# Kernel optimization log

Measured on AMD Instinct MI355X. Metric: run time of the kernel, lower is better.

The kernel has to match this reference:

```python
import jax, jax.numpy as jnp
import numpy as np

N = 100000
E = 1600000
F_IN = 128
F_OUT = 128


def setup_inputs() -> dict:
    key = jax.random.key(0)
    k1, k2, k3, k4, k5, k6 = jax.random.split(key, 6)
    stdv = 1.0 / np.sqrt(F_OUT)
    x = jax.random.normal(k1, (N, F_IN), dtype=jnp.float32)
    edge_row = jax.random.randint(k2, (E,), 0, N, dtype=jnp.int32)
    edge_col = jax.random.randint(k3, (E,), 0, N, dtype=jnp.int32)
    edge_val = jax.random.uniform(k4, (E,), dtype=jnp.float32)
    weight = jax.random.uniform(k5, (F_IN, F_OUT), minval=-stdv, maxval=stdv, dtype=jnp.float32)
    bias = jax.random.uniform(k6, (F_OUT,), minval=-stdv, maxval=stdv, dtype=jnp.float32)
    return {"x": x, "edge_row": edge_row, "edge_col": edge_col,
            "edge_val": edge_val, "weight": weight, "bias": bias}


def reference(x, edge_row, edge_col, edge_val, weight, bias):
    # support = X @ W  -> [N, F_OUT]
    support = jnp.matmul(x, weight)
    # sparse adjacency matmul: out[i] = sum_{e: row[e]==i} val[e] * support[col[e]]
    messages = edge_val[:, None] * support[edge_col]  # [E, F_OUT]
    out = jax.ops.segment_sum(messages, edge_row, num_segments=N)
    return out + bias
```

## Files before the change

### kernel.cpp

```cpp
#include <hip/hip_runtime.h>

#define FDIM 128
#define RPB  128
#define LOG_RPB 7
#define CAP  2560
#define TILE 8192
#define NTHR 256
#define NB_MAX 1024

typedef __attribute__((ext_vector_type(8))) short short8;
typedef __attribute__((ext_vector_type(4))) float f32x4;

__device__ inline unsigned pack_bf16x2(float a, float b) {
    unsigned ua = __float_as_uint(a);
    unsigned ub = __float_as_uint(b);
    ua += 0x7fffu + ((ua >> 16) & 1u);
    ub += 0x7fffu + ((ub >> 16) & 1u);
    return (ua >> 16) | (ub & 0xffff0000u);
}

__global__ __launch_bounds__(256) void w_prep(const float* __restrict__ W,
                                              uint4* __restrict__ Wsw,
                                              int* __restrict__ gfill, int nb) {
    const int id = blockIdx.x * 256 + threadIdx.x;
    if (id < nb) gfill[id] = id * CAP;
    const int c    = id & 127;
    const int kblk = id >> 7;
    unsigned u[4];
#pragma unroll
    for (int h = 0; h < 4; ++h) {
        float f0 = W[(size_t)(kblk * 8 + 2 * h) * FDIM + c];
        float f1 = W[(size_t)(kblk * 8 + 2 * h + 1) * FDIM + c];
        u[h] = pack_bf16x2(f0, f1);
    }
    Wsw[c * 16 + (kblk ^ (c & 7))] = make_uint4(u[0], u[1], u[2], u[3]);
}

__global__ __launch_bounds__(256) void gemm_mfma(const float* __restrict__ X,
                                                 const uint4* __restrict__ Wsw,
                                                 unsigned* __restrict__ Sb, int N) {
    __shared__ uint4 Wl[2048];
    const int t = threadIdx.x;
#pragma unroll
    for (int s = 0; s < 8; ++s) Wl[t + 256 * s] = Wsw[t + 256 * s];
    __syncthreads();

    const int w    = t >> 6;
    const int lane = t & 63;
    const int g    = lane >> 4;
    const int rl   = lane & 15;
    const int row  = blockIdx.x * 64 + 16 * w + rl;

    short8 bfrag[4];
    if (row < N) {
        const float4* X4 = (const float4*)(X + (size_t)row * FDIM);
#pragma unroll
        for (int kk = 0; kk < 4; ++kk) {
            float4 a = X4[kk * 8 + 2 * g];
            float4 b = X4[kk * 8 + 2 * g + 1];
            union { unsigned u[4]; short8 s; } f;
            f.u[0] = pack_bf16x2(a.x, a.y);
            f.u[1] = pack_bf16x2(a.z, a.w);
            f.u[2] = pack_bf16x2(b.x, b.y);
            f.u[3] = pack_bf16x2(b.z, b.w);
            bfrag[kk] = f.s;
        }
    } else {
        union { unsigned u[4]; short8 s; } z;
        z.u[0] = z.u[1] = z.u[2] = z.u[3] = 0;
#pragma unroll
        for (int kk = 0; kk < 4; ++kk) bfrag[kk] = z.s;
    }

    const short8* Wl8 = (const short8*)Wl;
    f32x4 acc[8] = {};
#pragma unroll
    for (int kk = 0; kk < 4; ++kk) {
#pragma unroll
        for (int ct = 0; ct < 8; ++ct) {
            const int c = ct * 16 + rl;
            short8 af = Wl8[c * 16 + ((kk * 4 + g) ^ (c & 7))];
            acc[ct] = __builtin_amdgcn_mfma_f32_16x16x32_bf16(af, bfrag[kk],
                                                              acc[ct], 0, 0, 0);
        }
    }

    if (row < N) {
#pragma unroll
        for (int ct = 0; ct < 8; ++ct) {
            unsigned u0 = pack_bf16x2(acc[ct][0], acc[ct][1]);
            unsigned u1 = pack_bf16x2(acc[ct][2], acc[ct][3]);
            *(uint2*)(Sb + (size_t)row * 64 + ct * 8 + 2 * g) = make_uint2(u0, u1);
        }
    }
}

__global__ __launch_bounds__(256) void binned_scatter(const int* __restrict__ erow,
                                                      const int* __restrict__ ecol,
                                                      const float* __restrict__ eval,
                                                      int* __restrict__ gfill,
                                                      int2* __restrict__ pairs,
                                                      int E, int nb) {
    __shared__ int lcnt[NB_MAX];
    __shared__ int rsv[NB_MAX];
    const int base = blockIdx.x * TILE;
    const int n = min(TILE, E - base);

    for (int i = threadIdx.x; i < nb; i += NTHR) lcnt[i] = 0;
    __syncthreads();

    for (int i = threadIdx.x; i < n; i += NTHR)
        atomicAdd(&lcnt[erow[base + i] >> LOG_RPB], 1);
    __syncthreads();

    for (int b = threadIdx.x; b < nb; b += NTHR) {
        int c = lcnt[b];
        rsv[b] = c ? atomicAdd(&gfill[b], c) : 0;
        lcnt[b] = 0;
    }
    __syncthreads();

    for (int i = threadIdx.x; i < n; i += NTHR) {
        int r = erow[base + i];
        int b = r >> LOG_RPB;
        int slot = rsv[b] + atomicAdd(&lcnt[b], 1);
        if (slot < b * CAP + CAP)
            pairs[slot] = make_int2(ecol[base + i] | ((r & (RPB - 1)) << 17),
                                    __float_as_int(eval[base + i]));
    }
}

__device__ inline void fma8(float* acc, float v, uint4 s) {
    acc[0] += v * __uint_as_float(s.x << 16);
    acc[1] += v * __uint_as_float(s.x & 0xffff0000u);
    acc[2] += v * __uint_as_float(s.y << 16);
    acc[3] += v * __uint_as_float(s.y & 0xffff0000u);
    acc[4] += v * __uint_as_float(s.z << 16);
    acc[5] += v * __uint_as_float(s.z & 0xffff0000u);
    acc[6] += v * __uint_as_float(s.w << 16);
    acc[7] += v * __uint_as_float(s.w & 0xffff0000u);
}

__global__ __launch_bounds__(512) void bucket_gather(const int* __restrict__ gfill,
                                                     const int2* __restrict__ pairs,
                                                     const uint4* __restrict__ Sb4,
                                                     const float* __restrict__ bias,
                                                     float* __restrict__ out, int N) {
    __shared__ int2 stage[CAP];
    __shared__ unsigned cp[CAP];
    __shared__ int lh[RPB], lx[RPB], lf[RPB], rs[RPB], re[RPB];
    const int b   = blockIdx.x;
    const int gb  = b * CAP;
    const int tid = threadIdx.x;
    const int cnt = min(gfill[b] - gb, CAP);

    for (int i = tid; i < cnt; i += 512) stage[i] = pairs[gb + i];
    if (tid < RPB) lh[tid] = 0;
    __syncthreads();

    for (int i = tid; i < cnt; i += 512)
        atomicAdd(&lh[(stage[i].x >> 17) & (RPB - 1)], 1);
    __syncthreads();

    if (tid < RPB) lx[tid] = lh[tid];
    __syncthreads();
    for (int off = 1; off < RPB; off <<= 1) {
        int y = 0;
        if (tid < RPB && tid >= off) y = lx[tid - off];
        __syncthreads();
        if (tid < RPB) lx[tid] += y;
        __syncthreads();
    }
    if (tid < RPB) {
        int excl = lx[tid] - lh[tid];
        rs[tid] = excl;
        re[tid] = lx[tid];
        lf[tid] = excl;
    }
    __syncthreads();

    for (int i = tid; i < cnt; i += 512) {
        int2 p = stage[i];
        int rl = (p.x >> 17) & (RPB - 1);
        int pos = atomicAdd(&lf[rl], 1);
        int q = __float2int_rn(__int_as_float(p.y) * 32768.f);
        q = min(max(q, 0), 32767);
        cp[pos] = (unsigned)(p.x & 0x1FFFF) | ((unsigned)q << 17);
    }
    __syncthreads();

    const int wid  = tid >> 6;
    const int lane = tid & 63;
    const int q    = lane >> 4;
    const int sl   = lane & 15;
    const float ISC = 1.f / 32768.f;
    const int row0 = b * RPB;

    for (int rr = 0; rr < 16; ++rr) {
        const int rl  = wid * 16 + rr;
        const int row = row0 + rl;
        if (row >= N) break;
        const int beg = rs[rl];
        const int end = re[rl];
        float acc[8] = {};

        int j = beg;
        for (; j + 8 <= end; j += 8) {
            unsigned p0 = cp[j + q];
            unsigned p1 = cp[j + 4 + q];
            uint4 s0 = Sb4[(size_t)(p0 & 0x1FFFF) * 16 + sl];
            uint4 s1 = Sb4[(size_t)(p1 & 0x1FFFF) * 16 + sl];
            float v0 = (float)(p0 >> 17) * ISC;
            float v1 = (float)(p1 >> 17) * ISC;
            fma8(acc, v0, s0);
            fma8(acc, v1, s1);
        }
        for (; j < end; j += 4) {
            unsigned p = (j + q < end) ? cp[j + q] : 0u;
            uint4 s = Sb4[(size_t)(p & 0x1FFFF) * 16 + sl];
            float v = (float)(p >> 17) * ISC;
            fma8(acc, v, s);
        }

#pragma unroll
        for (int i = 0; i < 8; ++i) {
            acc[i] += __shfl_xor(acc[i], 16, 64);
            acc[i] += __shfl_xor(acc[i], 32, 64);
        }

        if (q == 0) {
            const float4* bi = (const float4*)(bias + sl * 8);
            float4 b0 = bi[0], b1 = bi[1];
            float4* o = (float4*)(out + (size_t)row * FDIM + sl * 8);
            o[0] = make_float4(acc[0] + b0.x, acc[1] + b0.y,
                               acc[2] + b0.z, acc[3] + b0.w);
            o[1] = make_float4(acc[4] + b1.x, acc[5] + b1.y,
                               acc[6] + b1.z, acc[7] + b1.w);
        }
    }
}

__global__ __launch_bounds__(256) void init_bias(float* __restrict__ out,
                                                 const float* __restrict__ bias,
                                                 int total4) {
    const float4* b4 = (const float4*)bias;
    float4* o4 = (float4*)out;
    for (int i = blockIdx.x * blockDim.x + threadIdx.x; i < total4;
         i += gridDim.x * blockDim.x)
        o4[i] = b4[i & 31];
}

__global__ __launch_bounds__(256) void scatter_edges(const int* __restrict__ erow,
                                                     const int* __restrict__ ecol,
                                                     const float* __restrict__ eval,
                                                     const unsigned* __restrict__ Sb,
                                                     float* __restrict__ out, int E) {
    const int g    = threadIdx.x >> 5;
    const int lane = threadIdx.x & 31;
    for (long long e = (long long)blockIdx.x * 8 + g; e < E;
         e += (long long)gridDim.x * 8) {
        const int   r = erow[e];
        const int   c = ecol[e];
        const float v = eval[e];
        uint2 u = *(const uint2*)(Sb + (size_t)c * 64 + lane * 2);
        float* o = out + (size_t)r * FDIM + lane * 4;
        atomicAdd(o + 0, v * __uint_as_float(u.x << 16));
        atomicAdd(o + 1, v * __uint_as_float(u.x & 0xffff0000u));
        atomicAdd(o + 2, v * __uint_as_float(u.y << 16));
        atomicAdd(o + 3, v * __uint_as_float(u.y & 0xffff0000u));
    }
}

extern "C" void kernel_launch(void* const* d_in, const int* in_sizes, int n_in,
                              void* d_out, int out_size, void* d_ws, size_t ws_size,
                              hipStream_t stream) {
    const float* x      = (const float*)d_in[0];
    const int*   erow   = (const int*)d_in[1];
    const int*   ecol   = (const int*)d_in[2];
    const float* eval   = (const float*)d_in[3];
    const float* weight = (const float*)d_in[4];
    const float* bias   = (const float*)d_in[5];
    float* out = (float*)d_out;

    const int N = in_sizes[0] / FDIM;
    const int E = in_sizes[1];
    const int nb = (N + RPB - 1) / RPB;

    char* ws = (char*)d_ws;
    const size_t WSW_BYTES  = 32768;
    const size_t S_BYTES    = (size_t)N * FDIM * 2;
    const size_t GF_BYTES   = ((size_t)nb * 4 + 255) & ~255ull;
    const size_t PAIR_BYTES = (size_t)nb * CAP * 8;
    const size_t NEED = WSW_BYTES + S_BYTES + GF_BYTES + PAIR_BYTES;

    uint4*    Wsw   = (uint4*)ws;
    unsigned* Sb    = (unsigned*)(ws + WSW_BYTES);
    int*      gfill = (int*)(ws + WSW_BYTES + S_BYTES);
    int2*     pairs = (int2*)(ws + WSW_BYTES + S_BYTES + GF_BYTES);

    const bool fast = (ws_size >= NEED && nb <= NB_MAX);

    w_prep<<<8, 256, 0, stream>>>(weight, Wsw, fast ? gfill : (int*)Sb, fast ? nb : 0);
    gemm_mfma<<<(N + 63) / 64, 256, 0, stream>>>(x, Wsw, Sb, N);

    if (fast) {
        binned_scatter<<<(E + TILE - 1) / TILE, NTHR, 0, stream>>>(erow, ecol, eval,
                                                                   gfill, pairs, E, nb);
        bucket_gather<<<nb, 512, 0, stream>>>(gfill, pairs, (const uint4*)Sb,
                                              bias, out, N);
    } else {
        init_bias<<<2048, 256, 0, stream>>>(out, bias, N * 32);
        scatter_edges<<<8192, 256, 0, stream>>>(erow, ecol, eval, Sb, out, E);
    }
}
```

Before: 129.7 us.

## Merge GEMM and edge binning scatter into one heterogeneous kernel launch

```diff
diff --git a/kernel.cpp b/kernel.cpp
--- a/kernel.cpp
+++ b/kernel.cpp
@@ -5,7 +5,6 @@
 #define LOG_RPB 7
 #define CAP  2560
 #define TILE 8192
-#define NTHR 256
 #define NB_MAX 1024
 
 typedef __attribute__((ext_vector_type(8))) short short8;
@@ -36,97 +35,99 @@
     Wsw[c * 16 + (kblk ^ (c & 7))] = make_uint4(u[0], u[1], u[2], u[3]);
 }
 
-__global__ __launch_bounds__(256) void gemm_mfma(const float* __restrict__ X,
-                                                 const uint4* __restrict__ Wsw,
-                                                 unsigned* __restrict__ Sb, int N) {
-    __shared__ uint4 Wl[2048];
+__global__ __launch_bounds__(256) void gemm_scatter(
+        const float* __restrict__ X, const uint4* __restrict__ Wsw,
+        unsigned* __restrict__ Sb, int N,
+        const int* __restrict__ erow, const int* __restrict__ ecol,
+        const float* __restrict__ eval,
+        int* __restrict__ gfill, int2* __restrict__ pairs, int E, int nb,
+        int nsb) {
+    __shared__ int shm[8192];
     const int t = threadIdx.x;
-#pragma unroll
-    for (int s = 0; s < 8; ++s) Wl[t + 256 * s] = Wsw[t + 256 * s];
-    __syncthreads();
-
-    const int w    = t >> 6;
-    const int lane = t & 63;
-    const int g    = lane >> 4;
-    const int rl   = lane & 15;
-    const int row  = blockIdx.x * 64 + 16 * w + rl;
-
-    short8 bfrag[4];
-    if (row < N) {
-        const float4* X4 = (const float4*)(X + (size_t)row * FDIM);
+
+    if ((int)blockIdx.x < nsb) {
+        int* lcnt = shm;
+        int* rsv  = shm + NB_MAX;
+        const int base = blockIdx.x * TILE;
+        const int n = min(TILE, E - base);
+
+        for (int i = t; i < nb; i += 256) lcnt[i] = 0;
+        __syncthreads();
+
+        for (int i = t; i < n; i += 256)
+            atomicAdd(&lcnt[erow[base + i] >> LOG_RPB], 1);
+        __syncthreads();
+
+        for (int b = t; b < nb; b += 256) {
+            int c = lcnt[b];
+            rsv[b] = c ? atomicAdd(&gfill[b], c) : 0;
+            lcnt[b] = 0;
+        }
+        __syncthreads();
+
+        for (int i = t; i < n; i += 256) {
+            int r = erow[base + i];
+            int b = r >> LOG_RPB;
+            int slot = rsv[b] + atomicAdd(&lcnt[b], 1);
+            if (slot < b * CAP + CAP)
+                pairs[slot] = make_int2(ecol[base + i] | ((r & (RPB - 1)) << 17),
+                                        __float_as_int(eval[base + i]));
+        }
+    } else {
+        uint4* Wl = (uint4*)shm;
+        const int bid = blockIdx.x - nsb;
+#pragma unroll
+        for (int s = 0; s < 8; ++s) Wl[t + 256 * s] = Wsw[t + 256 * s];
+        __syncthreads();
+
+        const int w    = t >> 6;
+        const int lane = t & 63;
+        const int g    = lane >> 4;
+        const int rl   = lane & 15;
+        const int row  = bid * 64 + 16 * w + rl;
+
+        short8 bfrag[4];
+        if (row < N) {
+            const float4* X4 = (const float4*)(X + (size_t)row * FDIM);
+#pragma unroll
+            for (int kk = 0; kk < 4; ++kk) {
+                float4 a = X4[kk * 8 + 2 * g];
+                float4 b = X4[kk * 8 + 2 * g + 1];
+                union { unsigned u[4]; short8 s; } f;
+                f.u[0] = pack_bf16x2(a.x, a.y);
+                f.u[1] = pack_bf16x2(a.z, a.w);
+                f.u[2] = pack_bf16x2(b.x, b.y);
+                f.u[3] = pack_bf16x2(b.z, b.w);
+                bfrag[kk] = f.s;
+            }
+        } else {
+            union { unsigned u[4]; short8 s; } z;
+            z.u[0] = z.u[1] = z.u[2] = z.u[3] = 0;
+#pragma unroll
+            for (int kk = 0; kk < 4; ++kk) bfrag[kk] = z.s;
+        }
+
+        const short8* Wl8 = (const short8*)Wl;
+        f32x4 acc[8] = {};
 #pragma unroll
         for (int kk = 0; kk < 4; ++kk) {
-            float4 a = X4[kk * 8 + 2 * g];
-            float4 b = X4[kk * 8 + 2 * g + 1];
-            union { unsigned u[4]; short8 s; } f;
-            f.u[0] = pack_bf16x2(a.x, a.y);
-            f.u[1] = pack_bf16x2(a.z, a.w);
-            f.u[2] = pack_bf16x2(b.x, b.y);
-            f.u[3] = pack_bf16x2(b.z, b.w);
-            bfrag[kk] = f.s;
-        }
-    } else {
-        union { unsigned u[4]; short8 s; } z;
-        z.u[0] = z.u[1] = z.u[2] = z.u[3] = 0;
-#pragma unroll
-        for (int kk = 0; kk < 4; ++kk) bfrag[kk] = z.s;
-    }
-
-    const short8* Wl8 = (const short8*)Wl;
-    f32x4 acc[8] = {};
-#pragma unroll
-    for (int kk = 0; kk < 4; ++kk) {
-#pragma unroll
-        for (int ct = 0; ct < 8; ++ct) {
-            const int c = ct * 16 + rl;
-            short8 af = Wl8[c * 16 + ((kk * 4 + g) ^ (c & 7))];
-            acc[ct] = __builtin_amdgcn_mfma_f32_16x16x32_bf16(af, bfrag[kk],
-                                                              acc[ct], 0, 0, 0);
-        }
-    }
-
-    if (row < N) {
-#pragma unroll
-        for (int ct = 0; ct < 8; ++ct) {
-            unsigned u0 = pack_bf16x2(acc[ct][0], acc[ct][1]);
-            unsigned u1 = pack_bf16x2(acc[ct][2], acc[ct][3]);
-            *(uint2*)(Sb + (size_t)row * 64 + ct * 8 + 2 * g) = make_uint2(u0, u1);
-        }
-    }
-}
-
-__global__ __launch_bounds__(256) void binned_scatter(const int* __restrict__ erow,
-                                                      const int* __restrict__ ecol,
-                                                      const float* __restrict__ eval,
-                                                      int* __restrict__ gfill,
-                                                      int2* __restrict__ pairs,
-                                                      int E, int nb) {
-    __shared__ int lcnt[NB_MAX];
-    __shared__ int rsv[NB_MAX];
-    const int base = blockIdx.x * TILE;
-    const int n = min(TILE, E - base);
-
-    for (int i = threadIdx.x; i < nb; i += NTHR) lcnt[i] = 0;
-    __syncthreads();
-
-    for (int i = threadIdx.x; i < n; i += NTHR)
-        atomicAdd(&lcnt[erow[base + i] >> LOG_RPB], 1);
-    __syncthreads();
-
-    for (int b = threadIdx.x; b < nb; b += NTHR) {
-        int c = lcnt[b];
-        rsv[b] = c ? atomicAdd(&gfill[b], c) : 0;
-        lcnt[b] = 0;
-    }
-    __syncthreads();
-
-    for (int i = threadIdx.x; i < n; i += NTHR) {
-        int r = erow[base + i];
-        int b = r >> LOG_RPB;
-        int slot = rsv[b] + atomicAdd(&lcnt[b], 1);
-        if (slot < b * CAP + CAP)
-            pairs[slot] = make_int2(ecol[base + i] | ((r & (RPB - 1)) << 17),
-                                    __float_as_int(eval[base + i]));
+#pragma unroll
+            for (int ct = 0; ct < 8; ++ct) {
+                const int c = ct * 16 + rl;
+                short8 af = Wl8[c * 16 + ((kk * 4 + g) ^ (c & 7))];
+                acc[ct] = __builtin_amdgcn_mfma_f32_16x16x32_bf16(af, bfrag[kk],
+                                                                  acc[ct], 0, 0, 0);
+            }
+        }
+
+        if (row < N) {
+#pragma unroll
+            for (int ct = 0; ct < 8; ++ct) {
+                unsigned u0 = pack_bf16x2(acc[ct][0], acc[ct][1]);
+                unsigned u1 = pack_bf16x2(acc[ct][2], acc[ct][3]);
+                *(uint2*)(Sb + (size_t)row * 64 + ct * 8 + 2 * g) = make_uint2(u0, u1);
+            }
+        }
     }
 }
 
@@ -301,14 +302,19 @@
     const bool fast = (ws_size >= NEED && nb <= NB_MAX);
 
     w_prep<<<8, 256, 0, stream>>>(weight, Wsw, fast ? gfill : (int*)Sb, fast ? nb : 0);
-    gemm_mfma<<<(N + 63) / 64, 256, 0, stream>>>(x, Wsw, Sb, N);
 
     if (fast) {
-        binned_scatter<<<(E + TILE - 1) / TILE, NTHR, 0, stream>>>(erow, ecol, eval,
-                                                                   gfill, pairs, E, nb);
+        const int nsb = (E + TILE - 1) / TILE;
+        const int ngb = (N + 63) / 64;
+        gemm_scatter<<<nsb + ngb, 256, 0, stream>>>(x, Wsw, Sb, N,
+                                                    erow, ecol, eval,
+                                                    gfill, pairs, E, nb, nsb);
         bucket_gather<<<nb, 512, 0, stream>>>(gfill, pairs, (const uint4*)Sb,
                                               bias, out, N);
     } else {
+        gemm_scatter<<<(N + 63) / 64, 256, 0, stream>>>(x, Wsw, Sb, N,
+                                                        erow, ecol, eval,
+                                                        (int*)Sb, (int2*)Sb, E, nb, 0);
         init_bias<<<2048, 256, 0, stream>>>(out, bias, N * 32);
         scatter_edges<<<8192, 256, 0, stream>>>(erow, ecol, eval, Sb, out, E);
     }
```

New measurement: 123.1 us. -5.0%, faster.
